# Kernel optimization log

Measured on AMD Instinct MI355X. Metric: run time of the kernel, lower is better.

The kernel has to match this reference:

```python
import jax, jax.numpy as jnp
import numpy as np

NUM_OBJECTS = 6          # self.NUM_OBJECTS
SCORE_THRESH = 1e-4      # self.score_tresh
NMS_THRESHS = jnp.asarray(np.arange(0.001, 1.0, 0.1), dtype=jnp.float32)  # 10 thresholds
K_CAND = 1024            # fixed-shape cap on (proposal,class) candidates per image
CLASS_OFFSET = 4096.0    # > max image coord; batched_nms per-class offset trick


def _iou_matrix(b):
    # b: [K,4] xyxy -> [K,K] IoU
    x1, y1, x2, y2 = b[:, 0], b[:, 1], b[:, 2], b[:, 3]
    area = (x2 - x1) * (y2 - y1)
    iw = jnp.clip(jnp.minimum(x2[:, None], x2[None, :]) - jnp.maximum(x1[:, None], x1[None, :]), 0.0)
    ih = jnp.clip(jnp.minimum(y2[:, None], y2[None, :]) - jnp.maximum(y1[:, None], y1[None, :]), 0.0)
    inter = iw * ih
    union = area[:, None] + area[None, :] - inter
    return jnp.where(union > 0, inter / union, 0.0)


def _greedy_nms(iou, valid, thresh):
    # candidates are pre-sorted by descending score; sequential greedy suppression
    K = valid.shape[0]
    ar = jnp.arange(K)
    def body(i, keep):
        sup = keep[i] & (iou[i] > thresh) & (ar > i)
        return keep & ~sup
    return jax.lax.fori_loop(0, K, body, valid)


def _per_image(logits, boxes, feats, hw):
    # logits [N,81], boxes [N,80,4], feats [N,2048], hw [2] (h,w)
    C = boxes.shape[1]
    probs = jax.nn.softmax(logits, axis=-1)[:, :C]          # drop background class
    h = hw[0].astype(boxes.dtype)
    w = hw[1].astype(boxes.dtype)
    b = jnp.stack([jnp.clip(boxes[..., 0], 0.0, w),         # clip to image
                   jnp.clip(boxes[..., 1], 0.0, h),
                   jnp.clip(boxes[..., 2], 0.0, w),
                   jnp.clip(boxes[..., 3], 0.0, h)], axis=-1)
    scores = probs.reshape(-1)                              # [N*C]
    vals, idx = jax.lax.top_k(jnp.where(scores > SCORE_THRESH, scores, -1.0), K_CAND)
    cand_valid = vals > SCORE_THRESH
    cb = b.reshape(-1, 4)[idx]                              # [K,4]
    cls = (idx % C).astype(boxes.dtype)
    prop = idx // C                                         # proposal row index
    iou = _iou_matrix(cb + cls[:, None] * CLASS_OFFSET)     # per-class NMS via offsets
    keeps = jax.vmap(lambda t: _greedy_nms(iou, cand_valid, t))(NMS_THRESHS)  # [T,K]
    counts = keeps.sum(axis=1)
    # torch loop: break at first (smallest) thresh yielding len(ids)==6, i.e. >=6 kept
    ok = counts >= NUM_OBJECTS
    t_sel = jnp.where(jnp.any(ok), jnp.argmax(ok), NMS_THRESHS.shape[0] - 1)
    keep = keeps[t_sel]
    _, top = jax.lax.top_k(jnp.where(keep, vals, -jnp.inf), NUM_OBJECTS)
    ids = prop[top]                                         # [6]
    return feats[ids].T                                     # [2048, 6] (permute(1,0))


def _forward(cls_logits, boxes, feature_pooled, image_hw):
    return jax.vmap(_per_image)(cls_logits, boxes, feature_pooled, image_hw)  # [B,2048,6]


def setup_inputs() -> dict:
    key = jax.random.key(0)
    k1, k2, k3, k4, k5 = jax.random.split(key, 5)
    B, N, C, D = 8, 1000, 80, 2048
    cls_logits = jax.random.normal(k1, (B, N, C + 1), dtype=jnp.float32)
    ctr = jax.random.uniform(k2, (B, N, C, 2), minval=0.0, maxval=800.0)
    sz = jax.random.uniform(k3, (B, N, C, 2), minval=8.0, maxval=200.0)
    boxes = jnp.concatenate([ctr - sz * 0.5, ctr + sz * 0.5], axis=-1).astype(jnp.float32)
    feature_pooled = jax.random.normal(k4, (B, N, D), dtype=jnp.float32)
    image_hw = jax.random.randint(k5, (B, 2), 600, 800, dtype=jnp.int32)
    return {"cls_logits": cls_logits, "boxes": boxes,
            "feature_pooled": feature_pooled, "image_hw": image_hw}


def reference(cls_logits, boxes, feature_pooled, image_hw):
    return _forward(cls_logits, boxes, feature_pooled, image_hw)
```

## Files before the change

kernel.cpp:

```cpp
#include <hip/hip_runtime.h>
#include <cmath>
#include <cstdint>

#define NB 8
#define NPROP 1000
#define NCLS 80
#define NLOG 81
#define KCAND 1024
#define NTH 10
#define DFEAT 2048
#define NOBJ 6
#define NSCORE (NPROP*NCLS)
#define HBLK 8
#define HCHUNK (NSCORE/HBLK)
#define PCHUNK (NPROP/HBLK)
#define CCAP 64
#define GMAX 2048
#define CPB (NCLS/HBLK)

constexpr size_t OFF_SCORES = 0;
constexpr size_t OFF_H1     = OFF_SCORES + (size_t)NB * NSCORE * 4;
constexpr size_t OFF_H2     = OFF_H1 + (size_t)NB * HBLK * 2048 * 4;
constexpr size_t OFF_CBUF   = OFF_H2 + (size_t)NB * HBLK * 2048 * 4;
constexpr size_t OFF_GCNT   = OFF_CBUF + (size_t)NB * GMAX * 8;
constexpr size_t OFF_S1P    = OFF_GCNT + (size_t)NB * 4096 * 4;
constexpr size_t OFF_S2P    = OFF_S1P + (size_t)NB * 2048 * 4;
constexpr size_t OFF_PIV    = OFF_S2P + (size_t)NB * 2048 * 4;
constexpr size_t OFF_CPROP  = OFF_PIV + (size_t)NB * 8 * 4;
constexpr size_t OFF_KEEPS  = OFF_CPROP + (size_t)NB * KCAND * 4;

__device__ __forceinline__ float nms_th(int t) {
    return (float)(0.001 + 0.1 * (double)t);
}

__device__ __forceinline__ unsigned score_vkey(float v) {
    float vv = (v > 1e-4f) ? v : -1.0f;
    unsigned bits = __float_as_uint(vv);
    unsigned u = (bits & 0x80000000u) ? ~bits : (bits | 0x80000000u);
    return ~u;
}

__device__ __forceinline__ void scan2048(unsigned a, unsigned b, unsigned* pre,
                                         unsigned K, int* out_b, int* out_rem) {
    __shared__ unsigned wsum[16];
    int tid = threadIdx.x;
    unsigned p = a + b;
    unsigned x = p;
    #pragma unroll
    for (int d = 1; d < 64; d <<= 1) {
        unsigned y = __shfl_up(x, (unsigned)d, 64);
        if ((tid & 63) >= d) x += y;
    }
    if ((tid & 63) == 63) wsum[tid >> 6] = x;
    __syncthreads();
    if (tid < 16) {
        unsigned w = wsum[tid];
        #pragma unroll
        for (int d = 1; d < 16; d <<= 1) {
            unsigned y = __shfl_up(w, (unsigned)d, 64);
            if (tid >= d) w += y;
        }
        wsum[tid] = w;
    }
    __syncthreads();
    unsigned wex = (tid >= 64) ? wsum[(tid >> 6) - 1] : 0u;
    unsigned E = x + wex - p;
    pre[2 * tid]     = E;
    pre[2 * tid + 1] = E + a;
    if (E < K && E + a >= K)              { *out_b = 2 * tid;     *out_rem = (int)(K - E); }
    else if (E + a < K && E + a + b >= K) { *out_b = 2 * tid + 1; *out_rem = (int)(K - (E + a)); }
}

__global__ __launch_bounds__(1024) void k_softhist(const float* __restrict__ logits,
                                                   float* __restrict__ scores,
                                                   unsigned* __restrict__ hist1) {
    __shared__ unsigned hh[2048];
    int img = blockIdx.x >> 3, blk = blockIdx.x & 7;
    int tid = threadIdx.x, wid = tid >> 6, lane = tid & 63;
    hh[tid] = 0; hh[tid + 1024] = 0;
    __syncthreads();
    for (int p = wid; p < PCHUNK; p += 16) {
        int prop = blk * PCHUNK + p;
        const float* L = logits + ((size_t)img * NPROP + prop) * NLOG;
        float l0 = L[lane];
        float l1 = (lane < 17) ? L[64 + lane] : -INFINITY;
        float m = fmaxf(l0, l1);
        #pragma unroll
        for (int o = 32; o > 0; o >>= 1) m = fmaxf(m, __shfl_xor(m, o, 64));
        float e0 = expf(l0 - m);
        float e1 = (lane < 17) ? expf(l1 - m) : 0.f;
        float s = e0 + e1;
        #pragma unroll
        for (int o = 32; o > 0; o >>= 1) s += __shfl_xor(s, o, 64);
        float* op = scores + ((size_t)img * NPROP + prop) * NCLS;
        float p0 = e0 / s;
        op[lane] = p0;
        atomicAdd(&hh[score_vkey(p0) >> 21], 1u);
        if (lane < 16) {
            float p1 = e1 / s;
            op[64 + lane] = p1;
            atomicAdd(&hh[score_vkey(p1) >> 21], 1u);
        }
    }
    __syncthreads();
    unsigned* outp = hist1 + ((size_t)img * HBLK + blk) * 2048;
    outp[tid] = hh[tid];
    outp[tid + 1024] = hh[tid + 1024];
}

__global__ __launch_bounds__(1024) void k_hist2p(const float* __restrict__ scores,
                                                 const unsigned* __restrict__ hist1,
                                                 unsigned* __restrict__ hist2,
                                                 unsigned* __restrict__ gcg) {
    __shared__ unsigned hh[2048];
    __shared__ int sb, sr;
    int img = blockIdx.x >> 3, blk = blockIdx.x & 7;
    int tid = threadIdx.x;
    if (tid < 512) gcg[img * 4096 + blk * 512 + tid] = 0;
    if (tid == 0) { sb = 0; sr = 1; }
    __syncthreads();
    {
        unsigned a1 = 0, b1v = 0;
        const unsigned* h1 = hist1 + (size_t)img * HBLK * 2048;
        #pragma unroll
        for (int s = 0; s < HBLK; ++s) {
            a1  += h1[s * 2048 + 2 * tid];
            b1v += h1[s * 2048 + 2 * tid + 1];
        }
        scan2048(a1, b1v, hh, KCAND, &sb, &sr);
    }
    __syncthreads();
    hh[tid] = 0; hh[tid + 1024] = 0;
    __syncthreads();
    unsigned b1 = (unsigned)sb & 2047u;
    const float4* sc4 = (const float4*)(scores + (size_t)img * NSCORE + (size_t)blk * HCHUNK);
    #define H2S(val) { unsigned vk = score_vkey(val); \
                       if ((vk >> 21) == b1) atomicAdd(&hh[(vk >> 10) & 2047u], 1u); }
    for (int e4 = tid; e4 < HCHUNK / 4; e4 += 1024) {
        float4 v = sc4[e4];
        H2S(v.x) H2S(v.y) H2S(v.z) H2S(v.w)
    }
    #undef H2S
    __syncthreads();
    unsigned* outp = hist2 + ((size_t)img * HBLK + blk) * 2048;
    outp[tid] = hh[tid];
    outp[tid + 1024] = hh[tid + 1024];
}

__global__ __launch_bounds__(1024) void k_gatherp(const float* __restrict__ scores,
                                                  const unsigned* __restrict__ hist1,
                                                  const unsigned* __restrict__ hist2,
                                                  unsigned long long* __restrict__ cbuf,
                                                  unsigned* __restrict__ gcg,
                                                  unsigned* __restrict__ s1pg,
                                                  unsigned* __restrict__ s2pg,
                                                  int* __restrict__ piv,
                                                  unsigned long long* __restrict__ keeps) {
    __shared__ unsigned s1p[2048];
    __shared__ unsigned s2p[2048];
    __shared__ int sb1, sr1, sb2, sr2;
    int img = blockIdx.x >> 3, blk = blockIdx.x & 7;
    int tid = threadIdx.x;
    if (blockIdx.x == 1) {
        for (int k = tid; k < NB * NTH * 16; k += 1024) keeps[k] = 0ULL;
    }
    if (tid == 0) { sb1 = 0; sr1 = 1; sb2 = 0; sr2 = 1; }
    __syncthreads();
    {
        unsigned a1 = 0, b1v = 0;
        const unsigned* h1 = hist1 + (size_t)img * HBLK * 2048;
        #pragma unroll
        for (int s = 0; s < HBLK; ++s) {
            a1  += h1[s * 2048 + 2 * tid];
            b1v += h1[s * 2048 + 2 * tid + 1];
        }
        scan2048(a1, b1v, s1p, KCAND, &sb1, &sr1);
    }
    __syncthreads();
    {
        unsigned a2 = 0, b2v = 0;
        const unsigned* h2 = hist2 + (size_t)img * HBLK * 2048;
        #pragma unroll
        for (int s = 0; s < HBLK; ++s) {
            a2  += h2[s * 2048 + 2 * tid];
            b2v += h2[s * 2048 + 2 * tid + 1];
        }
        scan2048(a2, b2v, s2p, (unsigned)sr1, &sb2, &sr2);
    }
    __syncthreads();
    unsigned b1 = (unsigned)sb1 & 2047u;
    unsigned sb2m = (unsigned)sb2 & 2047u;
    unsigned T22 = (b1 << 11) | sb2m;
    const float4* sc4 = (const float4*)(scores + (size_t)img * NSCORE + (size_t)blk * HCHUNK);
    unsigned long long* cb = cbuf + (size_t)img * GMAX;
    unsigned* gc = gcg + img * 4096;
    #define GAS(val, ei) { unsigned vk = score_vkey(val); unsigned t22 = vk >> 10; \
        if (t22 <= T22) { \
            unsigned h = vk >> 21; unsigned g, base; \
            if (h == b1) { unsigned sub = t22 & 2047u; g = 2048u + sub; base = s1p[b1] + s2p[sub]; } \
            else         { g = h;                      base = s1p[h]; } \
            unsigned slot = atomicAdd(&gc[g], 1u); \
            unsigned posn = base + slot; \
            if (posn < GMAX) cb[posn] = ((unsigned long long)vk << 32) | (unsigned)(ei); } }
    for (int e4 = tid; e4 < HCHUNK / 4; e4 += 1024) {
        float4 v = sc4[e4];
        int e = blk * HCHUNK + 4 * e4;
        GAS(v.x, e) GAS(v.y, e + 1) GAS(v.z, e + 2) GAS(v.w, e + 3)
    }
    #undef GAS
    if (blk == 0) {
        s1pg[img * 2048 + tid] = s1p[tid];
        s1pg[img * 2048 + tid + 1024] = s1p[tid + 1024];
        s2pg[img * 2048 + tid] = s2p[tid];
        s2pg[img * 2048 + tid + 1024] = s2p[tid + 1024];
        if (tid == 0) { piv[img * 8 + 0] = sb1; piv[img * 8 + 4] = sb2; }
    }
}

__global__ __launch_bounds__(1024) void k_rnms(const unsigned long long* __restrict__ cbuf,
                                               const unsigned* __restrict__ gcg,
                                               const unsigned* __restrict__ s1pg,
                                               const unsigned* __restrict__ s2pg,
                                               const int* __restrict__ piv,
                                               const float* __restrict__ boxes,
                                               const int* __restrict__ hw,
                                               int* __restrict__ cprop,
                                               unsigned long long* __restrict__ keeps) {
    __shared__ unsigned s1p[2048];
    __shared__ unsigned s2p[2048];
    __shared__ unsigned long long keys[GMAX];
    __shared__ float scx1[KCAND], scy1[KCAND], scx2[KCAND], scy2[KCAND], scar[KCAND];
    __shared__ int   scprop[KCAND];
    __shared__ int   sclist[CPB * CCAP];
    __shared__ int   sccnt[CPB];
    __shared__ unsigned long long svalid[16];
    int img = blockIdx.x >> 3, sl = blockIdx.x & 7;
    int tid = threadIdx.x;

    scprop[tid] = 0;
    if (tid < CPB) sccnt[tid] = 0;
    if (tid < 16) svalid[tid] = 0ULL;
    s1p[tid] = s1pg[img * 2048 + tid];
    s1p[tid + 1024] = s1pg[img * 2048 + tid + 1024];
    s2p[tid] = s2pg[img * 2048 + tid];
    s2p[tid + 1024] = s2pg[img * 2048 + tid + 1024];
    __syncthreads();

    unsigned b1   = (unsigned)piv[img * 8 + 0] & 2047u;
    unsigned sb2m = (unsigned)piv[img * 8 + 4] & 2047u;
    const unsigned* gc = gcg + img * 4096;
    const unsigned long long* cb = cbuf + (size_t)img * GMAX;
    int cnt = (int)(s1p[b1] + s2p[sb2m] + gc[2048u + sb2m]);
    if (cnt > GMAX || cnt < 0) cnt = GMAX;
    #pragma unroll
    for (int k = 0; k < 2; ++k) {
        int t = k * 1024 + tid;
        keys[t] = (t < cnt) ? cb[t] : ~0ULL;
    }
    __syncthreads();

    for (int p = tid; p < cnt; p += 1024) {
        unsigned long long akey = keys[p];
        unsigned vk = (unsigned)(akey >> 32);
        unsigned h = vk >> 21;
        unsigned base, gsz;
        if (h == b1) {
            unsigned sub = (vk >> 10) & 2047u;
            base = s1p[b1] + s2p[sub];
            gsz  = gc[2048u + sub];
        } else {
            base = s1p[h];
            gsz  = gc[h];
        }
        unsigned r_ = base;
        unsigned qe = base + gsz;
        if (qe > (unsigned)GMAX) qe = (unsigned)GMAX;
        #pragma unroll 4
        for (unsigned q = base; q < qe; ++q)
            r_ += (keys[q] < akey) ? 1u : 0u;
        int r = (int)r_;
        unsigned idx = (unsigned)akey;
        int prop = (int)(idx / NCLS);
        if (r >= 0 && r < KCAND && (unsigned)prop < NPROP) {
            unsigned u = ~vk;
            const unsigned uth = __float_as_uint(1e-4f) | 0x80000000u;
            bool valid = u > uth;
            int cls = (int)(idx - (unsigned)prop * NCLS);
            const float4 bx = *(const float4*)(boxes + ((((size_t)img * NPROP + prop) * NCLS + cls) << 2));
            float fh = (float)hw[img * 2 + 0];
            float fw = (float)hw[img * 2 + 1];
            float x1 = fminf(fmaxf(bx.x, 0.f), fw);
            float y1 = fminf(fmaxf(bx.y, 0.f), fh);
            float x2 = fminf(fmaxf(bx.z, 0.f), fw);
            float y2 = fminf(fmaxf(bx.w, 0.f), fh);
            float offc = __fmul_rn((float)cls, 4096.0f);
            x1 = __fadd_rn(x1, offc); y1 = __fadd_rn(y1, offc);
            x2 = __fadd_rn(x2, offc); y2 = __fadd_rn(y2, offc);
            float area = __fmul_rn(__fsub_rn(x2, x1), __fsub_rn(y2, y1));
            scx1[r] = x1; scy1[r] = y1; scx2[r] = x2; scy2[r] = y2;
            scar[r] = area; scprop[r] = prop;
            if (valid) atomicOr(&svalid[r >> 6], 1ULL << (r & 63));
            int lc = cls - sl * CPB;
            if (lc >= 0 && lc < CPB) {
                int slot = atomicAdd(&sccnt[lc], 1);
                if (slot < CCAP) sclist[lc * CCAP + slot] = r;
            }
        }
    }
    __syncthreads();

    if (sl == 0) cprop[img * KCAND + tid] = scprop[tid];

    {
        int wv = tid >> 6, lane = tid & 63;
        if (wv < CPB) {
            int n = sccnt[wv];
            if (n > CCAP) n = CCAP;
            if (n > 0) {
                int rk = (lane < n) ? sclist[wv * CCAP + lane] : 0x7fffffff;
                int pos = 0;
                for (int j = 0; j < n; ++j) {
                    int rj = __shfl(rk, j, 64);
                    pos += (rj < rk) ? 1 : 0;
                }
                int srt = 0;
                for (int j = 0; j < n; ++j) {
                    int pj = __shfl(pos, j, 64);
                    int rj = __shfl(rk, j, 64);
                    if (pj == lane) srt = rj;
                }
                srt &= (KCAND - 1);
                bool act = lane < n;
                float x1 = 0, y1 = 0, x2 = 0, y2 = 0, ar = 0;
                bool val = false;
                if (act) {
                    x1 = scx1[srt]; y1 = scy1[srt];
                    x2 = scx2[srt]; y2 = scy2[srt]; ar = scar[srt];
                    val = (svalid[srt >> 6] >> (srt & 63)) & 1ULL;
                }
                unsigned long long m[NTH];
                #pragma unroll
                for (int t = 0; t < NTH; ++t) m[t] = 0ULL;
                for (int b = 0; b < n; ++b) {
                    float xj1 = __shfl(x1, b, 64), yj1 = __shfl(y1, b, 64);
                    float xj2 = __shfl(x2, b, 64), yj2 = __shfl(y2, b, 64);
                    float aj  = __shfl(ar, b, 64);
                    float iw = fmaxf(__fsub_rn(fminf(x2, xj2), fmaxf(x1, xj1)), 0.f);
                    float ih = fmaxf(__fsub_rn(fminf(y2, yj2), fmaxf(y1, yj1)), 0.f);
                    float inter = __fmul_rn(iw, ih);
                    float uni   = __fsub_rn(__fadd_rn(ar, aj), inter);
                    float iou   = (uni > 0.f) ? __fdiv_rn(inter, uni) : 0.f;
                    if (act && b < lane) {
                        #pragma unroll
                        for (int t = 0; t < NTH; ++t)
                            if (iou > nms_th(t)) m[t] |= 1ULL << b;
                    }
                }
                unsigned long long vmask = __ballot(act && val);
                for (int t = 0; t < NTH; ++t) {
                    unsigned long long keep = vmask;
                    for (int it = 0; it <= n; ++it) {
                        bool nk = act && val && ((m[t] & keep) == 0ULL);
                        unsigned long long nb = __ballot(nk);
                        if (nb == keep) break;
                        keep = nb;
                    }
                    if (act && ((keep >> lane) & 1ULL))
                        atomicOr(&keeps[((size_t)img * NTH + t) * 16 + (srt >> 6)], 1ULL << (srt & 63));
                }
            }
        }
    }
}

__global__ __launch_bounds__(256) void k_selfeat(const unsigned long long* __restrict__ keeps,
                                                 const int* __restrict__ cprop,
                                                 const float* __restrict__ feats,
                                                 float* __restrict__ outp) {
    __shared__ int scnt[NTH];
    __shared__ unsigned long long skw[16];
    __shared__ int stsel;
    __shared__ int sids[NOBJ];
    int img = blockIdx.x >> 3;
    int tid = threadIdx.x;
    if (tid < NTH) scnt[tid] = 0;
    __syncthreads();
    if (tid < NTH * 16) {
        unsigned long long w = keeps[(size_t)img * NTH * 16 + tid];
        int pc = __popcll(w);
        if (pc) atomicAdd(&scnt[tid >> 4], pc);
    }
    __syncthreads();
    if (tid == 0) {
        int tsel = NTH - 1;
        for (int t = 0; t < NTH; ++t) if (scnt[t] >= NOBJ) { tsel = t; break; }
        stsel = tsel;
    }
    __syncthreads();
    if (tid < 16) skw[tid] = keeps[((size_t)img * NTH + stsel) * 16 + tid];
    __syncthreads();
    if (tid == 0) {
        int got = 0;
        for (int k = 0; k < 16 && got < NOBJ; ++k) {
            unsigned long long x = skw[k];
            while (x && got < NOBJ) {
                int b = __builtin_ctzll(x);
                int sid = cprop[img * KCAND + k * 64 + b];
                sids[got++] = ((unsigned)sid < NPROP) ? sid : 0;
                x &= x - 1;
            }
        }
        for (int k = 0; k < 16 && got < NOBJ; ++k) {
            unsigned long long x = ~skw[k];
            while (x && got < NOBJ) {
                int b = __builtin_ctzll(x);
                int sid = cprop[img * KCAND + k * 64 + b];
                sids[got++] = ((unsigned)sid < NPROP) ? sid : 0;
                x &= x - 1;
            }
        }
    }
    __syncthreads();
    int d = (blockIdx.x & 7) * 256 + tid;
    const float* fb = feats + (size_t)img * NPROP * DFEAT;
    float* ob = outp + ((size_t)img * DFEAT + d) * NOBJ;
    #pragma unroll
    for (int s = 0; s < NOBJ; ++s)
        ob[s] = fb[(size_t)sids[s] * DFEAT + d];
}

extern "C" void kernel_launch(void* const* d_in, const int* in_sizes, int n_in,
                              void* d_out, int out_size, void* d_ws, size_t ws_size,
                              hipStream_t stream) {
    const float* logits = (const float*)d_in[0];
    const float* boxes  = (const float*)d_in[1];
    const float* feats  = (const float*)d_in[2];
    const int*   hw     = (const int*)d_in[3];
    float* outp = (float*)d_out;

    char* ws = (char*)d_ws;
    float*              scores = (float*)(ws + OFF_SCORES);
    unsigned*           hist1  = (unsigned*)(ws + OFF_H1);
    unsigned*           hist2  = (unsigned*)(ws + OFF_H2);
    unsigned long long* cbuf   = (unsigned long long*)(ws + OFF_CBUF);
    unsigned*           gcg    = (unsigned*)(ws + OFF_GCNT);
    unsigned*           s1pg   = (unsigned*)(ws + OFF_S1P);
    unsigned*           s2pg   = (unsigned*)(ws + OFF_S2P);
    int*                piv    = (int*)(ws + OFF_PIV);
    int*                cprop  = (int*)(ws + OFF_CPROP);
    unsigned long long* keeps  = (unsigned long long*)(ws + OFF_KEEPS);

    k_softhist<<<NB * HBLK, 1024, 0, stream>>>(logits, scores, hist1);
    k_hist2p<<<NB * HBLK, 1024, 0, stream>>>(scores, hist1, hist2, gcg);
    k_gatherp<<<NB * HBLK, 1024, 0, stream>>>(scores, hist1, hist2, cbuf, gcg,
                                              s1pg, s2pg, piv, keeps);
    k_rnms<<<NB * HBLK, 1024, 0, stream>>>(cbuf, gcg, s1pg, s2pg, piv, boxes, hw,
                                           cprop, keeps);
    k_selfeat<<<NB * HBLK, 256, 0, stream>>>(keeps, cprop, feats, outp);
}
```

Before: 149.9 us.

## Fuse per-class NMS and feature selection into one kernel, NMS redundantly per block

Merges the NMS kernel and the feature-gather kernel into one launch. Each of the 8 blocks per image now runs NMS for all 80 classes instead of its own 10-class slice, keeps the keep-masks and candidate-to-proposal map in shared memory, and gathers its slice of the output. This removes a kernel launch and the global round-trip of the keeps and proposal-index buffers. The cost is 8x redundant NMS work per image and a larger dynamic shared-memory footprint.

Result: slower. 190.9 us (+27.4%).

```diff
diff --git a/kernel.cpp b/kernel.cpp
--- a/kernel.cpp
+++ b/kernel.cpp
@@ -16,7 +16,6 @@
 #define PCHUNK (NPROP/HBLK)
 #define CCAP 64
 #define GMAX 2048
-#define CPB (NCLS/HBLK)
 
 constexpr size_t OFF_SCORES = 0;
 constexpr size_t OFF_H1     = OFF_SCORES + (size_t)NB * NSCORE * 4;
@@ -26,8 +25,21 @@
 constexpr size_t OFF_S1P    = OFF_GCNT + (size_t)NB * 4096 * 4;
 constexpr size_t OFF_S2P    = OFF_S1P + (size_t)NB * 2048 * 4;
 constexpr size_t OFF_PIV    = OFF_S2P + (size_t)NB * 2048 * 4;
-constexpr size_t OFF_CPROP  = OFF_PIV + (size_t)NB * 8 * 4;
-constexpr size_t OFF_KEEPS  = OFF_CPROP + (size_t)NB * KCAND * 4;
+
+constexpr int L_S1P   = 0;
+constexpr int L_S2P   = L_S1P + 8192;
+constexpr int L_KEYS  = L_S2P + 8192;
+constexpr int L_CX1   = L_KEYS + 16384;
+constexpr int L_CY1   = L_CX1 + 4096;
+constexpr int L_CX2   = L_CY1 + 4096;
+constexpr int L_CY2   = L_CX2 + 4096;
+constexpr int L_CAR   = L_CY2 + 4096;
+constexpr int L_CPROP = L_CAR + 4096;
+constexpr int L_CLIST = L_CPROP + 4096;
+constexpr int L_CCNT  = L_CLIST + 20480;
+constexpr int L_VALID = L_CCNT + 320;
+constexpr int L_KEEPS = L_VALID + 128;
+constexpr int SMEM4   = L_KEEPS + 1280;
 
 __device__ __forceinline__ float nms_th(int t) {
     return (float)(0.001 + 0.1 * (double)t);
@@ -154,16 +166,12 @@
                                                   unsigned* __restrict__ gcg,
                                                   unsigned* __restrict__ s1pg,
                                                   unsigned* __restrict__ s2pg,
-                                                  int* __restrict__ piv,
-                                                  unsigned long long* __restrict__ keeps) {
+                                                  int* __restrict__ piv) {
     __shared__ unsigned s1p[2048];
     __shared__ unsigned s2p[2048];
     __shared__ int sb1, sr1, sb2, sr2;
     int img = blockIdx.x >> 3, blk = blockIdx.x & 7;
     int tid = threadIdx.x;
-    if (blockIdx.x == 1) {
-        for (int k = tid; k < NB * NTH * 16; k += 1024) keeps[k] = 0ULL;
-    }
     if (tid == 0) { sb1 = 0; sr1 = 1; sb2 = 0; sr2 = 1; }
     __syncthreads();
     {
@@ -217,29 +225,42 @@
     }
 }
 
-__global__ __launch_bounds__(1024) void k_rnms(const unsigned long long* __restrict__ cbuf,
-                                               const unsigned* __restrict__ gcg,
-                                               const unsigned* __restrict__ s1pg,
-                                               const unsigned* __restrict__ s2pg,
-                                               const int* __restrict__ piv,
-                                               const float* __restrict__ boxes,
-                                               const int* __restrict__ hw,
-                                               int* __restrict__ cprop,
-                                               unsigned long long* __restrict__ keeps) {
-    __shared__ unsigned s1p[2048];
-    __shared__ unsigned s2p[2048];
-    __shared__ unsigned long long keys[GMAX];
-    __shared__ float scx1[KCAND], scy1[KCAND], scx2[KCAND], scy2[KCAND], scar[KCAND];
-    __shared__ int   scprop[KCAND];
-    __shared__ int   sclist[CPB * CCAP];
-    __shared__ int   sccnt[CPB];
-    __shared__ unsigned long long svalid[16];
+__global__ __launch_bounds__(1024) void k_tail4(const unsigned long long* __restrict__ cbuf,
+                                                const unsigned* __restrict__ gcg,
+                                                const unsigned* __restrict__ s1pg,
+                                                const unsigned* __restrict__ s2pg,
+                                                const int* __restrict__ piv,
+                                                const float* __restrict__ boxes,
+                                                const int* __restrict__ hw,
+                                                const float* __restrict__ feats,
+                                                float* __restrict__ outp) {
+    extern __shared__ char smem[];
+    unsigned* s1p   = (unsigned*)(smem + L_S1P);
+    unsigned* s2p   = (unsigned*)(smem + L_S2P);
+    unsigned long long* keys = (unsigned long long*)(smem + L_KEYS);
+    float* scx1     = (float*)(smem + L_CX1);
+    float* scy1     = (float*)(smem + L_CY1);
+    float* scx2     = (float*)(smem + L_CX2);
+    float* scy2     = (float*)(smem + L_CY2);
+    float* scar     = (float*)(smem + L_CAR);
+    int*   scprop   = (int*)(smem + L_CPROP);
+    int*   sclist   = (int*)(smem + L_CLIST);
+    int*   sccnt    = (int*)(smem + L_CCNT);
+    unsigned long long* svalid = (unsigned long long*)(smem + L_VALID);
+    unsigned long long* skeeps = (unsigned long long*)(smem + L_KEEPS);
+    __shared__ int scnt6[NTH];
+    __shared__ unsigned long long skw[16];
+    __shared__ int stsel;
+    __shared__ int sids[NOBJ];
+
     int img = blockIdx.x >> 3, sl = blockIdx.x & 7;
     int tid = threadIdx.x;
 
     scprop[tid] = 0;
-    if (tid < CPB) sccnt[tid] = 0;
+    if (tid < NCLS) sccnt[tid] = 0;
     if (tid < 16) svalid[tid] = 0ULL;
+    if (tid < NTH * 16) skeeps[tid] = 0ULL;
+    if (tid < NTH) scnt6[tid] = 0;
     s1p[tid] = s1pg[img * 2048 + tid];
     s1p[tid + 1024] = s1pg[img * 2048 + tid + 1024];
     s2p[tid] = s2pg[img * 2048 + tid];
@@ -300,104 +321,86 @@
             scx1[r] = x1; scy1[r] = y1; scx2[r] = x2; scy2[r] = y2;
             scar[r] = area; scprop[r] = prop;
             if (valid) atomicOr(&svalid[r >> 6], 1ULL << (r & 63));
-            int lc = cls - sl * CPB;
-            if (lc >= 0 && lc < CPB) {
-                int slot = atomicAdd(&sccnt[lc], 1);
-                if (slot < CCAP) sclist[lc * CCAP + slot] = r;
-            }
-        }
-    }
-    __syncthreads();
-
-    if (sl == 0) cprop[img * KCAND + tid] = scprop[tid];
+            int slot = atomicAdd(&sccnt[cls], 1);
+            if (slot < CCAP) sclist[cls * CCAP + slot] = r;
+        }
+    }
+    __syncthreads();
 
     {
         int wv = tid >> 6, lane = tid & 63;
-        if (wv < CPB) {
-            int n = sccnt[wv];
+        for (int cls = wv; cls < NCLS; cls += 16) {
+            int n = sccnt[cls];
             if (n > CCAP) n = CCAP;
-            if (n > 0) {
-                int rk = (lane < n) ? sclist[wv * CCAP + lane] : 0x7fffffff;
-                int pos = 0;
-                for (int j = 0; j < n; ++j) {
-                    int rj = __shfl(rk, j, 64);
-                    pos += (rj < rk) ? 1 : 0;
+            if (n == 0) continue;
+            int rk = (lane < n) ? sclist[cls * CCAP + lane] : 0x7fffffff;
+            int pos = 0;
+            for (int j = 0; j < n; ++j) {
+                int rj = __shfl(rk, j, 64);
+                pos += (rj < rk) ? 1 : 0;
+            }
+            int srt = 0;
+            for (int j = 0; j < n; ++j) {
+                int pj = __shfl(pos, j, 64);
+                int rj = __shfl(rk, j, 64);
+                if (pj == lane) srt = rj;
+            }
+            srt &= (KCAND - 1);
+            bool act = lane < n;
+            float x1 = 0, y1 = 0, x2 = 0, y2 = 0, ar = 0;
+            bool val = false;
+            if (act) {
+                x1 = scx1[srt]; y1 = scy1[srt];
+                x2 = scx2[srt]; y2 = scy2[srt]; ar = scar[srt];
+                val = (svalid[srt >> 6] >> (srt & 63)) & 1ULL;
+            }
+            unsigned long long m[NTH];
+            #pragma unroll
+            for (int t = 0; t < NTH; ++t) m[t] = 0ULL;
+            for (int b = 0; b < n; ++b) {
+                float xj1 = __shfl(x1, b, 64), yj1 = __shfl(y1, b, 64);
+                float xj2 = __shfl(x2, b, 64), yj2 = __shfl(y2, b, 64);
+                float aj  = __shfl(ar, b, 64);
+                float iw = fmaxf(__fsub_rn(fminf(x2, xj2), fmaxf(x1, xj1)), 0.f);
+                float ih = fmaxf(__fsub_rn(fminf(y2, yj2), fmaxf(y1, yj1)), 0.f);
+                float inter = __fmul_rn(iw, ih);
+                float uni   = __fsub_rn(__fadd_rn(ar, aj), inter);
+                float iou   = (uni > 0.f) ? __fdiv_rn(inter, uni) : 0.f;
+                if (act && b < lane) {
+                    #pragma unroll
+                    for (int t = 0; t < NTH; ++t)
+                        if (iou > nms_th(t)) m[t] |= 1ULL << b;
                 }
-                int srt = 0;
-                for (int j = 0; j < n; ++j) {
-                    int pj = __shfl(pos, j, 64);
-                    int rj = __shfl(rk, j, 64);
-                    if (pj == lane) srt = rj;
+            }
+            unsigned long long vmask = __ballot(act && val);
+            for (int t = 0; t < NTH; ++t) {
+                unsigned long long keep = vmask;
+                for (int it = 0; it <= n; ++it) {
+                    bool nk = act && val && ((m[t] & keep) == 0ULL);
+                    unsigned long long nb = __ballot(nk);
+                    if (nb == keep) break;
+                    keep = nb;
                 }
-                srt &= (KCAND - 1);
-                bool act = lane < n;
-                float x1 = 0, y1 = 0, x2 = 0, y2 = 0, ar = 0;
-                bool val = false;
-                if (act) {
-                    x1 = scx1[srt]; y1 = scy1[srt];
-                    x2 = scx2[srt]; y2 = scy2[srt]; ar = scar[srt];
-                    val = (svalid[srt >> 6] >> (srt & 63)) & 1ULL;
-                }
-                unsigned long long m[NTH];
-                #pragma unroll
-                for (int t = 0; t < NTH; ++t) m[t] = 0ULL;
-                for (int b = 0; b < n; ++b) {
-                    float xj1 = __shfl(x1, b, 64), yj1 = __shfl(y1, b, 64);
-                    float xj2 = __shfl(x2, b, 64), yj2 = __shfl(y2, b, 64);
-                    float aj  = __shfl(ar, b, 64);
-                    float iw = fmaxf(__fsub_rn(fminf(x2, xj2), fmaxf(x1, xj1)), 0.f);
-                    float ih = fmaxf(__fsub_rn(fminf(y2, yj2), fmaxf(y1, yj1)), 0.f);
-                    float inter = __fmul_rn(iw, ih);
-                    float uni   = __fsub_rn(__fadd_rn(ar, aj), inter);
-                    float iou   = (uni > 0.f) ? __fdiv_rn(inter, uni) : 0.f;
-                    if (act && b < lane) {
-                        #pragma unroll
-                        for (int t = 0; t < NTH; ++t)
-                            if (iou > nms_th(t)) m[t] |= 1ULL << b;
-                    }
-                }
-                unsigned long long vmask = __ballot(act && val);
-                for (int t = 0; t < NTH; ++t) {
-                    unsigned long long keep = vmask;
-                    for (int it = 0; it <= n; ++it) {
-                        bool nk = act && val && ((m[t] & keep) == 0ULL);
-                        unsigned long long nb = __ballot(nk);
-                        if (nb == keep) break;
-                        keep = nb;
-                    }
-                    if (act && ((keep >> lane) & 1ULL))
-                        atomicOr(&keeps[((size_t)img * NTH + t) * 16 + (srt >> 6)], 1ULL << (srt & 63));
-                }
-            }
-        }
-    }
-}
-
-__global__ __launch_bounds__(256) void k_selfeat(const unsigned long long* __restrict__ keeps,
-                                                 const int* __restrict__ cprop,
-                                                 const float* __restrict__ feats,
-                                                 float* __restrict__ outp) {
-    __shared__ int scnt[NTH];
-    __shared__ unsigned long long skw[16];
-    __shared__ int stsel;
-    __shared__ int sids[NOBJ];
-    int img = blockIdx.x >> 3;
-    int tid = threadIdx.x;
-    if (tid < NTH) scnt[tid] = 0;
-    __syncthreads();
+                if (act && ((keep >> lane) & 1ULL))
+                    atomicOr(&skeeps[t * 16 + (srt >> 6)], 1ULL << (srt & 63));
+            }
+        }
+    }
+    __syncthreads();
+
     if (tid < NTH * 16) {
-        unsigned long long w = keeps[(size_t)img * NTH * 16 + tid];
+        unsigned long long w = skeeps[tid];
         int pc = __popcll(w);
-        if (pc) atomicAdd(&scnt[tid >> 4], pc);
+        if (pc) atomicAdd(&scnt6[tid >> 4], pc);
     }
     __syncthreads();
     if (tid == 0) {
         int tsel = NTH - 1;
-        for (int t = 0; t < NTH; ++t) if (scnt[t] >= NOBJ) { tsel = t; break; }
+        for (int t = 0; t < NTH; ++t) if (scnt6[t] >= NOBJ) { tsel = t; break; }
         stsel = tsel;
     }
     __syncthreads();
-    if (tid < 16) skw[tid] = keeps[((size_t)img * NTH + stsel) * 16 + tid];
+    if (tid < 16) skw[tid] = skeeps[stsel * 16 + tid];
     __syncthreads();
     if (tid == 0) {
         int got = 0;
@@ -405,7 +408,7 @@
             unsigned long long x = skw[k];
             while (x && got < NOBJ) {
                 int b = __builtin_ctzll(x);
-                int sid = cprop[img * KCAND + k * 64 + b];
+                int sid = scprop[k * 64 + b];
                 sids[got++] = ((unsigned)sid < NPROP) ? sid : 0;
                 x &= x - 1;
             }
@@ -414,19 +417,20 @@
             unsigned long long x = ~skw[k];
             while (x && got < NOBJ) {
                 int b = __builtin_ctzll(x);
-                int sid = cprop[img * KCAND + k * 64 + b];
+                int sid = scprop[k * 64 + b];
                 sids[got++] = ((unsigned)sid < NPROP) ? sid : 0;
                 x &= x - 1;
             }
         }
     }
     __syncthreads();
-    int d = (blockIdx.x & 7) * 256 + tid;
+
     const float* fb = feats + (size_t)img * NPROP * DFEAT;
-    float* ob = outp + ((size_t)img * DFEAT + d) * NOBJ;
-    #pragma unroll
-    for (int s = 0; s < NOBJ; ++s)
-        ob[s] = fb[(size_t)sids[s] * DFEAT + d];
+    for (int t = tid; t < (DFEAT / HBLK) * NOBJ; t += 1024) {
+        int li = sl * ((DFEAT / HBLK) * NOBJ) + t;
+        int d = li / NOBJ, s = li - NOBJ * d;
+        outp[(size_t)img * (DFEAT * NOBJ) + li] = fb[(size_t)sids[s] * DFEAT + d];
+    }
 }
 
 extern "C" void kernel_launch(void* const* d_in, const int* in_sizes, int n_in,
@@ -447,14 +451,19 @@
     unsigned*           s1pg   = (unsigned*)(ws + OFF_S1P);
     unsigned*           s2pg   = (unsigned*)(ws + OFF_S2P);
     int*                piv    = (int*)(ws + OFF_PIV);
-    int*                cprop  = (int*)(ws + OFF_CPROP);
-    unsigned long long* keeps  = (unsigned long long*)(ws + OFF_KEEPS);
+
+    static bool attr_done = false;
+    if (!attr_done) {
+        (void)hipFuncSetAttribute(reinterpret_cast<const void*>(&k_tail4),
+                                  hipFuncAttributeMaxDynamicSharedMemorySize,
+                                  SMEM4);
+        attr_done = true;
+    }
 
     k_softhist<<<NB * HBLK, 1024, 0, stream>>>(logits, scores, hist1);
     k_hist2p<<<NB * HBLK, 1024, 0, stream>>>(scores, hist1, hist2, gcg);
     k_gatherp<<<NB * HBLK, 1024, 0, stream>>>(scores, hist1, hist2, cbuf, gcg,
-                                              s1pg, s2pg, piv, keeps);
-    k_rnms<<<NB * HBLK, 1024, 0, stream>>>(cbuf, gcg, s1pg, s2pg, piv, boxes, hw,
-                                           cprop, keeps);
-    k_selfeat<<<NB * HBLK, 256, 0, stream>>>(keeps, cprop, feats, outp);
-}
+                                              s1pg, s2pg, piv);
+    k_tail4<<<NB * HBLK, 1024, SMEM4, stream>>>(cbuf, gcg, s1pg, s2pg, piv,
+                                                boxes, hw, feats, outp);
+}
```

## Fuse feature selection into NMS kernel via last-block-done atomic counter

Applied to the files above, without the earlier changes.

Removes the separate k_selfeat launch. The last of the eight NMS blocks per image, detected with a global atomic counter, now picks the threshold, selects proposals from shared scprop and copies the features. This drops one kernel launch and the cprop global round trip. In exchange the gather for each image runs on a single 1024-thread block instead of eight blocks, and a memset is added to reset the counter.

Measured after the change: 154.7 us. 3.2% more time.

```diff
diff --git a/kernel.cpp b/kernel.cpp
--- a/kernel.cpp
+++ b/kernel.cpp
@@ -18,7 +18,8 @@
 #define GMAX 2048
 #define CPB (NCLS/HBLK)
 
-constexpr size_t OFF_SCORES = 0;
+constexpr size_t OFF_DONE   = 0;
+constexpr size_t OFF_SCORES = 256;
 constexpr size_t OFF_H1     = OFF_SCORES + (size_t)NB * NSCORE * 4;
 constexpr size_t OFF_H2     = OFF_H1 + (size_t)NB * HBLK * 2048 * 4;
 constexpr size_t OFF_CBUF   = OFF_H2 + (size_t)NB * HBLK * 2048 * 4;
@@ -26,8 +27,7 @@
 constexpr size_t OFF_S1P    = OFF_GCNT + (size_t)NB * 4096 * 4;
 constexpr size_t OFF_S2P    = OFF_S1P + (size_t)NB * 2048 * 4;
 constexpr size_t OFF_PIV    = OFF_S2P + (size_t)NB * 2048 * 4;
-constexpr size_t OFF_CPROP  = OFF_PIV + (size_t)NB * 8 * 4;
-constexpr size_t OFF_KEEPS  = OFF_CPROP + (size_t)NB * KCAND * 4;
+constexpr size_t OFF_KEEPS  = OFF_PIV + (size_t)NB * 8 * 4;
 
 __device__ __forceinline__ float nms_th(int t) {
     return (float)(0.001 + 0.1 * (double)t);
@@ -38,6 +38,10 @@
     unsigned bits = __float_as_uint(vv);
     unsigned u = (bits & 0x80000000u) ? ~bits : (bits | 0x80000000u);
     return ~u;
+}
+
+__device__ __forceinline__ unsigned long long cload_u64(const unsigned long long* p) {
+    return __hip_atomic_load((unsigned long long*)p, __ATOMIC_RELAXED, __HIP_MEMORY_SCOPE_AGENT);
 }
 
 __device__ __forceinline__ void scan2048(unsigned a, unsigned b, unsigned* pre,
@@ -224,8 +228,10 @@
                                                const int* __restrict__ piv,
                                                const float* __restrict__ boxes,
                                                const int* __restrict__ hw,
-                                               int* __restrict__ cprop,
-                                               unsigned long long* __restrict__ keeps) {
+                                               unsigned* __restrict__ done,
+                                               unsigned long long* __restrict__ keeps,
+                                               const float* __restrict__ feats,
+                                               float* __restrict__ outp) {
     __shared__ unsigned s1p[2048];
     __shared__ unsigned s2p[2048];
     __shared__ unsigned long long keys[GMAX];
@@ -234,12 +240,18 @@
     __shared__ int   sclist[CPB * CCAP];
     __shared__ int   sccnt[CPB];
     __shared__ unsigned long long svalid[16];
+    __shared__ int slast;
+    __shared__ int scnt6[NTH];
+    __shared__ unsigned long long skw[16];
+    __shared__ int stsel;
+    __shared__ int sids[NOBJ];
     int img = blockIdx.x >> 3, sl = blockIdx.x & 7;
     int tid = threadIdx.x;
 
     scprop[tid] = 0;
     if (tid < CPB) sccnt[tid] = 0;
     if (tid < 16) svalid[tid] = 0ULL;
+    if (tid < NTH) scnt6[tid] = 0;
     s1p[tid] = s1pg[img * 2048 + tid];
     s1p[tid + 1024] = s1pg[img * 2048 + tid + 1024];
     s2p[tid] = s2pg[img * 2048 + tid];
@@ -308,8 +320,6 @@
         }
     }
     __syncthreads();
-
-    if (sl == 0) cprop[img * KCAND + tid] = scprop[tid];
 
     {
         int wv = tid >> 6, lane = tid & 63;
@@ -371,33 +381,29 @@
             }
         }
     }
-}
-
-__global__ __launch_bounds__(256) void k_selfeat(const unsigned long long* __restrict__ keeps,
-                                                 const int* __restrict__ cprop,
-                                                 const float* __restrict__ feats,
-                                                 float* __restrict__ outp) {
-    __shared__ int scnt[NTH];
-    __shared__ unsigned long long skw[16];
-    __shared__ int stsel;
-    __shared__ int sids[NOBJ];
-    int img = blockIdx.x >> 3;
-    int tid = threadIdx.x;
-    if (tid < NTH) scnt[tid] = 0;
-    __syncthreads();
+    __syncthreads();
+    if (tid == 0) {
+        asm volatile("s_waitcnt vmcnt(0)" ::: "memory");
+        unsigned old = __hip_atomic_fetch_add(&done[img], 1u,
+                                              __ATOMIC_RELAXED, __HIP_MEMORY_SCOPE_AGENT);
+        slast = ((old & 7u) == 7u) ? 1 : 0;
+    }
+    __syncthreads();
+    if (!slast) return;
+
     if (tid < NTH * 16) {
-        unsigned long long w = keeps[(size_t)img * NTH * 16 + tid];
+        unsigned long long w = cload_u64(&keeps[(size_t)img * NTH * 16 + tid]);
         int pc = __popcll(w);
-        if (pc) atomicAdd(&scnt[tid >> 4], pc);
+        if (pc) atomicAdd(&scnt6[tid >> 4], pc);
     }
     __syncthreads();
     if (tid == 0) {
         int tsel = NTH - 1;
-        for (int t = 0; t < NTH; ++t) if (scnt[t] >= NOBJ) { tsel = t; break; }
+        for (int t = 0; t < NTH; ++t) if (scnt6[t] >= NOBJ) { tsel = t; break; }
         stsel = tsel;
     }
     __syncthreads();
-    if (tid < 16) skw[tid] = keeps[((size_t)img * NTH + stsel) * 16 + tid];
+    if (tid < 16) skw[tid] = cload_u64(&keeps[((size_t)img * NTH + stsel) * 16 + tid]);
     __syncthreads();
     if (tid == 0) {
         int got = 0;
@@ -405,7 +411,7 @@
             unsigned long long x = skw[k];
             while (x && got < NOBJ) {
                 int b = __builtin_ctzll(x);
-                int sid = cprop[img * KCAND + k * 64 + b];
+                int sid = scprop[k * 64 + b];
                 sids[got++] = ((unsigned)sid < NPROP) ? sid : 0;
                 x &= x - 1;
             }
@@ -414,19 +420,19 @@
             unsigned long long x = ~skw[k];
             while (x && got < NOBJ) {
                 int b = __builtin_ctzll(x);
-                int sid = cprop[img * KCAND + k * 64 + b];
+                int sid = scprop[k * 64 + b];
                 sids[got++] = ((unsigned)sid < NPROP) ? sid : 0;
                 x &= x - 1;
             }
         }
     }
     __syncthreads();
-    int d = (blockIdx.x & 7) * 256 + tid;
+
     const float* fb = feats + (size_t)img * NPROP * DFEAT;
-    float* ob = outp + ((size_t)img * DFEAT + d) * NOBJ;
-    #pragma unroll
-    for (int s = 0; s < NOBJ; ++s)
-        ob[s] = fb[(size_t)sids[s] * DFEAT + d];
+    for (int li = tid; li < DFEAT * NOBJ; li += 1024) {
+        int d = li / NOBJ, s = li - NOBJ * d;
+        outp[(size_t)img * (DFEAT * NOBJ) + li] = fb[(size_t)sids[s] * DFEAT + d];
+    }
 }
 
 extern "C" void kernel_launch(void* const* d_in, const int* in_sizes, int n_in,
@@ -439,6 +445,7 @@
     float* outp = (float*)d_out;
 
     char* ws = (char*)d_ws;
+    unsigned*           done   = (unsigned*)(ws + OFF_DONE);
     float*              scores = (float*)(ws + OFF_SCORES);
     unsigned*           hist1  = (unsigned*)(ws + OFF_H1);
     unsigned*           hist2  = (unsigned*)(ws + OFF_H2);
@@ -447,14 +454,13 @@
     unsigned*           s1pg   = (unsigned*)(ws + OFF_S1P);
     unsigned*           s2pg   = (unsigned*)(ws + OFF_S2P);
     int*                piv    = (int*)(ws + OFF_PIV);
-    int*                cprop  = (int*)(ws + OFF_CPROP);
     unsigned long long* keeps  = (unsigned long long*)(ws + OFF_KEEPS);
 
+    hipMemsetAsync(d_ws, 0, 64, stream);
     k_softhist<<<NB * HBLK, 1024, 0, stream>>>(logits, scores, hist1);
     k_hist2p<<<NB * HBLK, 1024, 0, stream>>>(scores, hist1, hist2, gcg);
     k_gatherp<<<NB * HBLK, 1024, 0, stream>>>(scores, hist1, hist2, cbuf, gcg,
                                               s1pg, s2pg, piv, keeps);
     k_rnms<<<NB * HBLK, 1024, 0, stream>>>(cbuf, gcg, s1pg, s2pg, piv, boxes, hw,
-                                           cprop, keeps);
-    k_selfeat<<<NB * HBLK, 256, 0, stream>>>(keeps, cprop, feats, outp);
-}
+                                           done, keeps, feats, outp);
+}
```
